# Kernel optimization log

Measured on AMD Instinct MI355X. Metric: run time of the kernel, lower is better.

The kernel has to match this reference:

```python
import jax, jax.numpy as jnp
import numpy as np

B, S, DIN, D, DOUT = 64, 128, 64, 1024, 64
NUM_ROTORS, NUM_REV = 3, 3


def setup_inputs() -> dict:
    key = jax.random.key(0)
    ks = jax.random.split(key, 12)
    s = 1.0 / np.sqrt(D)
    return {
        "x": jax.random.normal(ks[0], (B, S, DIN), jnp.float32),
        "Wi": jax.random.normal(ks[1], (D, DIN), jnp.float32) / np.sqrt(DIN),
        "bi": jnp.zeros((D,), jnp.float32),
        "P": jax.random.normal(ks[2], (D, D), jnp.float32) * s,          # plugboard
        "rotW": jax.random.normal(ks[3], (NUM_ROTORS, D, D), jnp.float32) * s,
        "F": jax.random.normal(ks[4], (NUM_REV, D // 2, D // 2), jnp.float32) * np.sqrt(2.0 / D),
        "G": jax.random.normal(ks[5], (NUM_REV, D // 2, D // 2), jnp.float32) * np.sqrt(2.0 / D),
        "R": jax.random.normal(ks[6], (D, D), jnp.float32) * (0.5 * s),  # reflector seed (symmetrized)
        "Wo": jax.random.normal(ks[7], (DOUT, D), jnp.float32) * s,
        "bo": jnp.zeros((DOUT,), jnp.float32),
    }


def _rev_block(h, f, g):
    # additive coupling (reversible block): split, couple, concat
    h1, h2 = jnp.split(h, 2, axis=-1)
    y1 = h1 + jnp.tanh(h2 @ f)
    y2 = h2 + jnp.tanh(y1 @ g)
    return jnp.concatenate([y1, y2], axis=-1)


def reference(x, Wi, bi, P, rotW, F, G, R, Wo, bo):
    d = Wi.shape[0]
    n_rot = rotW.shape[0]
    n_rev = F.shape[0]
    S_refl = R + R.T  # symmetric reflector

    def step(carry, inp):
        x_t, t = inp  # x_t: [B, DIN], t: scalar int32
        h = x_t @ Wi.T + bi                 # input projection
        h = h @ P.T                         # plugboard forward
        # rotors (odometer stepping: rotor i advances every d**i steps)
        for i in range(n_rot):
            pos = (t // (d ** i)) % d
            h = jnp.roll(jnp.roll(h, -pos, axis=-1) @ rotW[i], pos, axis=-1)
        for i in range(n_rev):
            h = _rev_block(h, F[i], G[i])
        h = h @ S_refl                      # reflector
        for i in reversed(range(n_rev)):
            h = _rev_block(h, F[i], G[i])
        for i in reversed(range(n_rot)):    # rotors inverse on return path
            pos = (t // (d ** i)) % d
            h = jnp.roll(jnp.roll(h, -pos, axis=-1) @ rotW[i].T, pos, axis=-1)
        h = h @ P                           # plugboard transpose
        return carry, h @ Wo.T + bo

    xs = (jnp.swapaxes(x, 0, 1), jnp.arange(x.shape[1], dtype=jnp.int32))
    _, outs = jax.lax.scan(step, 0, xs)     # outs: [S, B, DOUT]
    return jnp.swapaxes(outs, 0, 1)
```

## Files before the change

kernel.cpp:

```cpp
#include <hip/hip_runtime.h>
#include <math.h>

#define DD 1024
#define MM 8192
#define SS 128
#define DINN 64
#define DOUTN 64

typedef _Float16 f16;
typedef _Float16 f16x8 __attribute__((ext_vector_type(8)));
typedef _Float16 f16x4 __attribute__((ext_vector_type(4)));
typedef float    f32x4 __attribute__((ext_vector_type(4)));

#define GLOAD_LDS(g, l) \
  __builtin_amdgcn_global_load_lds((const __attribute__((address_space(1))) void*)(g), \
                                   (__attribute__((address_space(3))) void*)(l), 16, 0, 0)

template<int BM, bool EPI, int SHIFT>
__global__ __launch_bounds__(256)
void k_gemm16(const f16* __restrict__ A, int lda,
              const f16* __restrict__ B, int ldb,
              f16* __restrict__ C, int ldc, int K) {
  constexpr int MT = BM / 32;
  constexpr int AI = BM / 64;
  __shared__ f16 sA[2][BM * 32];
  __shared__ f16 sB[2][128 * 32];

  const int nwg = gridDim.x * gridDim.y;
  int wg = blockIdx.y * gridDim.x + blockIdx.x;
  wg = (wg & 7) * (nwg >> 3) + (wg >> 3);
  const int bx = wg % gridDim.x, by = wg / gridDim.x;

  const int col0 = bx * 128, row0 = by * BM;
  const int u = threadIdx.x, lane = u & 63, wv = u >> 6;
  const int mh = (wv >> 1) * (BM >> 1);
  const int nh = (wv & 1) * 64;

  unsigned aoff[AI], boff[2];
  unsigned dstA[AI], dstB[2];
#pragma unroll
  for (int i = 0; i < AI; ++i) {
    const int P = i * 256 + u;
    const int row = P >> 2, kc = (P & 3) ^ ((row >> 1) & 3);
    aoff[i] = (unsigned)(row0 + row) * lda + kc * 8;
    dstA[i] = (i * 256 + wv * 64) * 8;
  }
#pragma unroll
  for (int i = 0; i < 2; ++i) {
    const int P = i * 256 + u;
    const int row = P >> 2, kc = (P & 3) ^ ((row >> 1) & 3);
    boff[i] = (unsigned)(col0 + row) * ldb + kc * 8;
    dstB[i] = (i * 256 + wv * 64) * 8;
  }

  const int frag = (lane & 15) * 32 + (((lane >> 4) ^ ((lane >> 1) & 3)) * 8);

  f32x4 acc[MT][4];
#pragma unroll
  for (int i = 0; i < MT; ++i)
#pragma unroll
    for (int j = 0; j < 4; ++j) acc[i][j] = (f32x4){0.f, 0.f, 0.f, 0.f};

  auto stage = [&](int b, int k0) {
#pragma unroll
    for (int i = 0; i < AI; ++i)
      GLOAD_LDS(A + aoff[i] + k0, &sA[b][dstA[i]]);
#pragma unroll
    for (int i = 0; i < 2; ++i)
      GLOAD_LDS(B + boff[i] + k0, &sB[b][dstB[i]]);
  };

  const int niter = K >> 5;
  stage(0, 0);
  __syncthreads();

  int buf = 0;
  for (int it = 0; it < niter; ++it) {
    if (it + 1 < niter) stage(buf ^ 1, (it + 1) << 5);
    f16x8 aF[MT], bF[4];
#pragma unroll
    for (int mt = 0; mt < MT; ++mt)
      aF[mt] = *(const f16x8*)&sA[buf][(mh + mt * 16) * 32 + frag];
#pragma unroll
    for (int nt = 0; nt < 4; ++nt)
      bF[nt] = *(const f16x8*)&sB[buf][(nh + nt * 16) * 32 + frag];
#pragma unroll
    for (int mt = 0; mt < MT; ++mt)
#pragma unroll
      for (int nt = 0; nt < 4; ++nt)
        acc[mt][nt] = __builtin_amdgcn_mfma_f32_16x16x32_f16(aF[mt], bF[nt], acc[mt][nt], 0, 0, 0);
    __syncthreads();
    buf ^= 1;
  }

  if constexpr (SHIFT == 0) {
    f16* eH = &sB[0][0] + wv * (16 * 84);
    const int lrow4 = (lane >> 4) << 2;
    const int lcol = lane & 15;
#pragma unroll
    for (int mt = 0; mt < MT; ++mt) {
#pragma unroll
      for (int nt = 0; nt < 4; ++nt) {
        const f32x4 a = acc[mt][nt];
#pragma unroll
        for (int r = 0; r < 4; ++r)
          eH[(lrow4 + r) * 84 + nt * 16 + lcol] = (f16)a[r];
      }
#pragma unroll
      for (int j = 0; j < 2; ++j) {
        const int idx = j * 64 + lane;
        const int row = idx >> 3, ch = idx & 7;
        const f16x8 vh = *(const f16x8*)&eH[row * 84 + ch * 8];
        const int m = row0 + mh + mt * 16 + row;
        const size_t gi = (size_t)m * ldc + col0 + nh + ch * 8;
        if (EPI) {
          const f16x8 oh = *(const f16x8*)&C[gi];
          f16x8 rh;
#pragma unroll
          for (int q = 0; q < 8; ++q)
            rh[q] = (f16)((float)oh[q] + tanhf((float)vh[q]));
          *(f16x8*)&C[gi] = rh;
        } else {
          *(f16x8*)&C[gi] = vh;
        }
      }
    }
  } else {
#pragma unroll
    for (int mt = 0; mt < MT; ++mt)
#pragma unroll
      for (int nt = 0; nt < 4; ++nt) {
        const f32x4 a = acc[mt][nt];
        const int n_base = col0 + nh + nt * 16 + (lane & 15);
#pragma unroll
        for (int r = 0; r < 4; ++r) {
          const int m = row0 + mh + mt * 16 + ((lane >> 4) << 2) + r;
          int n = (n_base + SHIFT * (m >> 6) + 2048) & (DD - 1);
          const size_t idx = (size_t)m * ldc + n;
          float y = a[r];
          if (EPI) y = (float)C[idx] + tanhf(y);
          C[idx] = (f16)y;
        }
      }
  }
}

__global__ __launch_bounds__(256)
void k_in_mfma(const f16* __restrict__ xS,
               const f16* __restrict__ A2,
               const float* __restrict__ cvec,
               f16* __restrict__ hS) {
  __shared__ f16 sA[2][64 * 32];
  __shared__ f16 sB[2][128 * 32];
  const int bx = blockIdx.x, by = blockIdx.y;
  const int col0 = bx * 128, row0 = by * 64, t = by;
  const int u = threadIdx.x, lane = u & 63, wv = u >> 6;
  const int mh = (wv >> 1) * 32;
  const int nh = (wv & 1) * 64;

  unsigned aoff, boff[2], dstA, dstB[2];
  {
    const int row = u >> 2, kc = (u & 3) ^ ((row >> 1) & 3);
    aoff = (unsigned)(row * SS + t) * DINN + kc * 8;
    dstA = (unsigned)(wv * 64) * 8;
  }
#pragma unroll
  for (int i = 0; i < 2; ++i) {
    const int P = i * 256 + u;
    const int row = P >> 2, kc = (P & 3) ^ ((row >> 1) & 3);
    const int src = (col0 + row + t) & (DD - 1);
    boff[i] = (unsigned)src * DINN + kc * 8;
    dstB[i] = (i * 256 + wv * 64) * 8;
  }

  const int frag = (lane & 15) * 32 + (((lane >> 4) ^ ((lane >> 1) & 3)) * 8);

  f32x4 acc[2][4];
#pragma unroll
  for (int i = 0; i < 2; ++i)
#pragma unroll
    for (int j = 0; j < 4; ++j) acc[i][j] = (f32x4){0.f, 0.f, 0.f, 0.f};

  auto stage = [&](int b, int k0) {
    GLOAD_LDS(xS + aoff + k0, &sA[b][dstA]);
#pragma unroll
    for (int i = 0; i < 2; ++i)
      GLOAD_LDS(A2 + boff[i] + k0, &sB[b][dstB[i]]);
  };

  stage(0, 0);
  __syncthreads();
  int buf = 0;
#pragma unroll
  for (int it = 0; it < 2; ++it) {
    if (it == 0) stage(1, 32);
    f16x8 aF[2], bF[4];
#pragma unroll
    for (int mt = 0; mt < 2; ++mt)
      aF[mt] = *(const f16x8*)&sA[buf][(mh + mt * 16) * 32 + frag];
#pragma unroll
    for (int nt = 0; nt < 4; ++nt)
      bF[nt] = *(const f16x8*)&sB[buf][(nh + nt * 16) * 32 + frag];
#pragma unroll
    for (int mt = 0; mt < 2; ++mt)
#pragma unroll
      for (int nt = 0; nt < 4; ++nt)
        acc[mt][nt] = __builtin_amdgcn_mfma_f32_16x16x32_f16(aF[mt], bF[nt], acc[mt][nt], 0, 0, 0);
    __syncthreads();
    buf ^= 1;
  }

  f16* eH = &sB[0][0] + wv * (16 * 84);
  const int lrow4 = (lane >> 4) << 2;
  const int lcol = lane & 15;
#pragma unroll
  for (int mt = 0; mt < 2; ++mt) {
#pragma unroll
    for (int nt = 0; nt < 4; ++nt) {
      const f32x4 a = acc[mt][nt];
      const int n = col0 + nh + nt * 16 + lcol;
      const float cv = cvec[(n + t) & (DD - 1)];
#pragma unroll
      for (int r = 0; r < 4; ++r)
        eH[(lrow4 + r) * 84 + nt * 16 + lcol] = (f16)(a[r] + cv);
    }
#pragma unroll
    for (int j = 0; j < 2; ++j) {
      const int idx = j * 64 + lane;
      const int row = idx >> 3, ch = idx & 7;
      const f16x8 vh = *(const f16x8*)&eH[row * 84 + ch * 8];
      const int m = row0 + mh + mt * 16 + row;
      *(f16x8*)&hS[(size_t)m * DD + col0 + nh + ch * 8] = vh;
    }
  }
}

__global__ __launch_bounds__(256)
void k_out_mfma(const f16* __restrict__ A,
                const f16* __restrict__ B,
                const float* __restrict__ bo, float* __restrict__ out) {
  __shared__ f16 sA[2][64 * 32];
  __shared__ f16 sB[2][64 * 32];
  const int row0 = blockIdx.x * 64;
  const int u = threadIdx.x, lane = u & 63, wv = u >> 6;
  const int mh = (wv >> 1) * 32, nh = (wv & 1) * 32;

  const int srow = u >> 2, skc = (u & 3) ^ ((srow >> 1) & 3);
  const unsigned aoff = (unsigned)(row0 + srow) * DD + skc * 8;
  const unsigned boff = (unsigned)srow * DD + skc * 8;
  const unsigned dst = (unsigned)(wv * 64) * 8;

  const int frag = (lane & 15) * 32 + (((lane >> 4) ^ ((lane >> 1) & 3)) * 8);

  f32x4 acc[2][2];
#pragma unroll
  for (int i = 0; i < 2; ++i)
#pragma unroll
    for (int j = 0; j < 2; ++j) acc[i][j] = (f32x4){0.f, 0.f, 0.f, 0.f};

  auto stage = [&](int b, int k0) {
    GLOAD_LDS(A + aoff + k0, &sA[b][dst]);
    GLOAD_LDS(B + boff + k0, &sB[b][dst]);
  };

  stage(0, 0);
  __syncthreads();
  int buf = 0;
  for (int it = 0; it < 32; ++it) {
    if (it + 1 < 32) stage(buf ^ 1, (it + 1) << 5);
    f16x8 aF[2], bF[2];
#pragma unroll
    for (int mt = 0; mt < 2; ++mt)
      aF[mt] = *(const f16x8*)&sA[buf][(mh + mt * 16) * 32 + frag];
#pragma unroll
    for (int nt = 0; nt < 2; ++nt)
      bF[nt] = *(const f16x8*)&sB[buf][(nh + nt * 16) * 32 + frag];
#pragma unroll
    for (int mt = 0; mt < 2; ++mt)
#pragma unroll
      for (int nt = 0; nt < 2; ++nt)
        acc[mt][nt] = __builtin_amdgcn_mfma_f32_16x16x32_f16(aF[mt], bF[nt], acc[mt][nt], 0, 0, 0);
    __syncthreads();
    buf ^= 1;
  }

#pragma unroll
  for (int mt = 0; mt < 2; ++mt)
#pragma unroll
    for (int nt = 0; nt < 2; ++nt) {
      const f32x4 a = acc[mt][nt];
      const int c = nh + nt * 16 + (lane & 15);
      const float bias = bo[c];
#pragma unroll
      for (int r = 0; r < 4; ++r) {
        const int m = row0 + mh + mt * 16 + ((lane >> 4) << 2) + r;
        const int t = m >> 6, b = m & 63;
        out[((size_t)b * SS + t) * DOUTN + c] = a[r] + bias;
      }
    }
}

__global__ __launch_bounds__(256)
void k_cvt(const float* __restrict__ src, f16* __restrict__ dst) {
  const int i = blockIdx.x * 256 + threadIdx.x;
  const float4 v = ((const float4*)src)[i];
  f16x4 h4;
  h4[0] = (f16)v.x; h4[1] = (f16)v.y; h4[2] = (f16)v.z; h4[3] = (f16)v.w;
  ((f16x4*)dst)[i] = h4;
}

__global__ __launch_bounds__(256)
void k_cvtT(const float* __restrict__ src, f16* __restrict__ dst, int dim) {
  src += (size_t)blockIdx.z * dim * dim;
  dst += (size_t)blockIdx.z * dim * dim;
  const int i0 = blockIdx.y * 64, j0 = blockIdx.x * 64;
  __shared__ float tb[64][68];
  const int u = threadIdx.x;
#pragma unroll
  for (int it = 0; it < 4; ++it) {
    const int idx = it * 256 + u, rr = idx >> 4, cc = (idx & 15) * 4;
    *(float4*)&tb[rr][cc] = *(const float4*)&src[(size_t)(i0 + rr) * dim + j0 + cc];
  }
  __syncthreads();
#pragma unroll
  for (int it = 0; it < 4; ++it) {
    const int idx = it * 256 + u, rr = idx >> 4, cc = (idx & 15) * 4;
    f16x4 h4;
#pragma unroll
    for (int j = 0; j < 4; ++j) h4[j] = (f16)tb[cc + j][rr];
    *(f16x4*)&dst[(size_t)(j0 + rr) * dim + i0 + cc] = h4;
  }
}

__global__ __launch_bounds__(256)
void k_symm_cvt(const float* __restrict__ R, f16* __restrict__ S) {
  const int i0 = blockIdx.y * 64, j0 = blockIdx.x * 64;
  __shared__ float tb[64][68];
  const int u = threadIdx.x;
#pragma unroll
  for (int it = 0; it < 4; ++it) {
    const int idx = it * 256 + u, rr = idx >> 4, cc = (idx & 15) * 4;
    *(float4*)&tb[rr][cc] = *(const float4*)&R[(size_t)(j0 + rr) * DD + i0 + cc];
  }
  __syncthreads();
#pragma unroll
  for (int it = 0; it < 4; ++it) {
    const int idx = it * 256 + u, rr = idx >> 4, cc = (idx & 15) * 4;
    const float4 v = *(const float4*)&R[(size_t)(i0 + rr) * DD + j0 + cc];
    f16x4 h4;
    h4[0] = (f16)(v.x + tb[cc + 0][rr]); h4[1] = (f16)(v.y + tb[cc + 1][rr]);
    h4[2] = (f16)(v.z + tb[cc + 2][rr]); h4[3] = (f16)(v.w + tb[cc + 3][rr]);
    *(f16x4*)&S[(size_t)(i0 + rr) * DD + j0 + cc] = h4;
  }
}

__global__ __launch_bounds__(256)
void k_tr16(const f16* __restrict__ in, f16* __restrict__ o, int dim) {
  const int i0 = blockIdx.y * 64, j0 = blockIdx.x * 64;
  __shared__ f16 tb[64][72];
  const int u = threadIdx.x;
#pragma unroll
  for (int it = 0; it < 2; ++it) {
    const int C = it * 256 + u, row = C >> 3, ch = C & 7;
    *(f16x8*)&tb[row][ch * 8] = *(const f16x8*)&in[(size_t)(i0 + row) * dim + j0 + ch * 8];
  }
  __syncthreads();
#pragma unroll
  for (int it = 0; it < 2; ++it) {
    const int C = it * 256 + u, row = C >> 3, ch = C & 7;
    f16x8 v;
#pragma unroll
    for (int j = 0; j < 8; ++j) v[j] = tb[ch * 8 + j][row];
    *(f16x8*)&o[(size_t)(j0 + row) * dim + i0 + ch * 8] = v;
  }
}

__global__ __launch_bounds__(256)
void k_pwi(const float* __restrict__ P, const float* __restrict__ Wi,
           f16* __restrict__ A2) {
  const int m0 = blockIdx.x * 4;
  __shared__ float Ps[4][1024];
  const int u = threadIdx.x;
#pragma unroll
  for (int i = 0; i < 4; ++i) {
    const int idx = i * 256 + u, mi = idx >> 8, kc = (idx & 255) * 4;
    *(float4*)&Ps[mi][kc] = *(const float4*)&P[(size_t)(m0 + mi) * DD + kc];
  }
  __syncthreads();
  const int n = u & 63, mi = u >> 6;
  float acc = 0.f;
  for (int k = 0; k < DD; ++k) acc += Ps[mi][k] * Wi[(size_t)k * DINN + n];
  A2[(size_t)(m0 + mi) * DINN + n] = (f16)acc;
}

__global__ __launch_bounds__(256)
void k_pwo(const float* __restrict__ P, const float* __restrict__ Wo_,
           f16* __restrict__ MoT) {
  const int d0 = blockIdx.x * 4;
  __shared__ float Ps[4][1024];
  __shared__ float ws[64][65];
  const int u = threadIdx.x;
#pragma unroll
  for (int i = 0; i < 4; ++i) {
    const int idx = i * 256 + u, mi = idx >> 8, kc = (idx & 255) * 4;
    *(float4*)&Ps[mi][kc] = *(const float4*)&P[(size_t)(d0 + mi) * DD + kc];
  }
  const int c = u & 63, di = u >> 6;
  float acc = 0.f;
  for (int k0 = 0; k0 < DD; k0 += 64) {
    __syncthreads();
#pragma unroll
    for (int i = 0; i < 4; ++i) {
      const int idx = i * 256 + u, cc = idx >> 4, kc = (idx & 15) * 4;
      const float4 v = *(const float4*)&Wo_[(size_t)cc * DD + k0 + kc];
      ws[cc][kc] = v.x; ws[cc][kc + 1] = v.y; ws[cc][kc + 2] = v.z; ws[cc][kc + 3] = v.w;
    }
    __syncthreads();
    for (int kk = 0; kk < 64; ++kk) acc += Ps[di][k0 + kk] * ws[c][kk];
  }
  MoT[(size_t)c * DD + d0 + di] = (f16)acc;
}

__global__ __launch_bounds__(256)
void k_matvec(const float* __restrict__ P, const float* __restrict__ b,
              float* __restrict__ c) {
  const int row = blockIdx.x * 4 + (threadIdx.x >> 6);
  const int l = threadIdx.x & 63;
  float s = 0.f;
  for (int k = l; k < DD; k += 64) s += P[(size_t)row * DD + k] * b[k];
  for (int o = 32; o; o >>= 1) s += __shfl_down(s, o, 64);
  if (l == 0) c[row] = s;
}

extern "C" void kernel_launch(void* const* d_in, const int* in_sizes, int n_in,
                              void* d_out, int out_size, void* d_ws, size_t ws_size,
                              hipStream_t stream) {
  (void)in_sizes; (void)n_in; (void)out_size; (void)ws_size;
  const float* x    = (const float*)d_in[0];
  const float* Wi   = (const float*)d_in[1];
  const float* bi   = (const float*)d_in[2];
  const float* P    = (const float*)d_in[3];
  const float* rotW = (const float*)d_in[4];
  const float* F    = (const float*)d_in[5];
  const float* G    = (const float*)d_in[6];
  const float* R    = (const float*)d_in[7];
  const float* Wo   = (const float*)d_in[8];
  const float* bo   = (const float*)d_in[9];
  float* out = (float*)d_out;
  char* w = (char*)d_ws;

  constexpr size_t MB = 1u << 20;
  f16* haS = (f16*)(w + 0 * MB);
  f16* hbS = (f16*)(w + 16 * MB);
  f16* B0t = (f16*)(w + 32 * MB);
  f16* B12t= (f16*)(w + 34 * MB);
  f16* Bss = (f16*)(w + 36 * MB);
  f16* B12 = (f16*)(w + 38 * MB);
  f16* B0  = (f16*)(w + 40 * MB);
  f16* BF  = (f16*)(w + 42 * MB);
  f16* BG  = (f16*)(w + 44 * MB);
  f16* MoT    = (f16*)(w + 46 * MB);
  f16* A2     = (f16*)(w + 46 * MB + 128 * 1024);
  float* cvec = (float*)(w + 46 * MB + 256 * 1024);
  f16* xs     = (f16*)(w + 47 * MB);
  f16* W1s = (f16*)(w + 48 * MB);
  f16* W2t = (f16*)(w + 50 * MB);

  const float* W0 = rotW;
  const float* W1 = rotW + (1u << 20);
  const float* W2 = rotW + (2u << 20);

  const dim3 blk256(256);
  const size_t FGQ = (size_t)512 * 512;

  k_cvt     <<<dim3(1024), blk256, 0, stream>>>(W1, W1s);
  k_cvtT    <<<dim3(16, 16), blk256, 0, stream>>>(W2, W2t, DD);
  k_gemm16<64, false, 0><<<dim3(8, 16), blk256, 0, stream>>>(W1s, DD, W2t, DD, B12, DD, DD);
  k_tr16    <<<dim3(16, 16), blk256, 0, stream>>>(B12, B12t, DD);
  k_symm_cvt<<<dim3(16, 16), blk256, 0, stream>>>(R, Bss);
  k_cvtT    <<<dim3(16, 16), blk256, 0, stream>>>(W0, B0t, DD);
  k_cvt     <<<dim3(1024), blk256, 0, stream>>>(W0, B0);
  k_cvtT    <<<dim3(8, 8, 3), blk256, 0, stream>>>(F, BF, 512);
  k_cvtT    <<<dim3(8, 8, 3), blk256, 0, stream>>>(G, BG, 512);
  k_cvt     <<<dim3(512), blk256, 0, stream>>>(x, xs);
  k_pwi     <<<dim3(256), blk256, 0, stream>>>(P, Wi, A2);
  k_pwo     <<<dim3(256), blk256, 0, stream>>>(P, Wo, MoT);
  k_matvec  <<<dim3(256), blk256, 0, stream>>>(P, bi, cvec);

  k_in_mfma<<<dim3(8, 128), blk256, 0, stream>>>(xs, A2, cvec, haS);

  k_gemm16<128, false, +1><<<dim3(8, 64), blk256, 0, stream>>>(haS, DD, B0t, DD, hbS, DD, DD);
  k_gemm16<128, false, 0><<<dim3(8, 64), blk256, 0, stream>>>(hbS, DD, B12t, DD, haS, DD, DD);
  for (int i = 0; i < 3; ++i) {
    k_gemm16<64, true, 0><<<dim3(4, 128), blk256, 0, stream>>>(haS + 512, DD, BF + i * FGQ, 512, haS, DD, 512);
    k_gemm16<64, true, 0><<<dim3(4, 128), blk256, 0, stream>>>(haS, DD, BG + i * FGQ, 512, haS + 512, DD, 512);
  }
  k_gemm16<128, false, 0><<<dim3(8, 64), blk256, 0, stream>>>(haS, DD, Bss, DD, hbS, DD, DD);
  for (int i = 2; i >= 0; --i) {
    k_gemm16<64, true, 0><<<dim3(4, 128), blk256, 0, stream>>>(hbS + 512, DD, BF + i * FGQ, 512, hbS, DD, 512);
    k_gemm16<64, true, 0><<<dim3(4, 128), blk256, 0, stream>>>(hbS, DD, BG + i * FGQ, 512, hbS + 512, DD, 512);
  }
  k_gemm16<128, false, -1><<<dim3(8, 64), blk256, 0, stream>>>(hbS, DD, B12, DD, haS, DD, DD);
  k_gemm16<128, false, +1><<<dim3(8, 64), blk256, 0, stream>>>(haS, DD, B0, DD, hbS, DD, DD);

  k_out_mfma<<<dim3(128), blk256, 0, stream>>>(hbS, MoT, bo, out);
}
```

Baseline: 419.8 us.

## Split-K the W1·W2 precompute, merge conversion kernels, shrink main GEMM tiles

Merges several fp32-to-fp16 conversion and transpose launches into fewer combined kernels, which cuts launch count in the weight-prep phase. Replaces the 128-block W1·W2 product with a 4-way split-K GEMM into fp32 partials plus a summing kernel, giving that step more parallelism. Also switches the main 1024-wide GEMMs from BM=128 to BM=64 tiles, doubling the block count (1024 blocks) to improve CU occupancy at the cost of reloading the B operand more often. The split-K path adds 16 MB of fp32 partial traffic.

```diff
diff --git a/kernel.cpp b/kernel.cpp
--- a/kernel.cpp
+++ b/kernel.cpp
@@ -143,6 +143,94 @@
         }
       }
   }
+}
+
+__global__ __launch_bounds__(256)
+void k_w12part(const f16* __restrict__ A, const f16* __restrict__ B,
+               float* __restrict__ Cp) {
+  __shared__ f16 sA[2][64 * 32];
+  __shared__ f16 sB[2][128 * 32];
+  const int kOff = blockIdx.z * 256;
+  float* Co = Cp + (size_t)blockIdx.z * DD * DD;
+  const int col0 = blockIdx.x * 128, row0 = blockIdx.y * 64;
+  const int u = threadIdx.x, lane = u & 63, wv = u >> 6;
+  const int mh = (wv >> 1) * 32, nh = (wv & 1) * 64;
+
+  unsigned aoff, boff[2], dstA, dstB[2];
+  {
+    const int row = u >> 2, kc = (u & 3) ^ ((row >> 1) & 3);
+    aoff = (unsigned)(row0 + row) * DD + kOff + kc * 8;
+    dstA = (unsigned)(wv * 64) * 8;
+  }
+#pragma unroll
+  for (int i = 0; i < 2; ++i) {
+    const int P = i * 256 + u;
+    const int row = P >> 2, kc = (P & 3) ^ ((row >> 1) & 3);
+    boff[i] = (unsigned)(col0 + row) * DD + kOff + kc * 8;
+    dstB[i] = (i * 256 + wv * 64) * 8;
+  }
+  const int frag = (lane & 15) * 32 + (((lane >> 4) ^ ((lane >> 1) & 3)) * 8);
+
+  f32x4 acc[2][4];
+#pragma unroll
+  for (int i = 0; i < 2; ++i)
+#pragma unroll
+    for (int j = 0; j < 4; ++j) acc[i][j] = (f32x4){0.f, 0.f, 0.f, 0.f};
+
+  auto stage = [&](int b, int k0) {
+    GLOAD_LDS(A + aoff + k0, &sA[b][dstA]);
+#pragma unroll
+    for (int i = 0; i < 2; ++i)
+      GLOAD_LDS(B + boff[i] + k0, &sB[b][dstB[i]]);
+  };
+
+  stage(0, 0);
+  __syncthreads();
+  int buf = 0;
+  for (int it = 0; it < 8; ++it) {
+    if (it + 1 < 8) stage(buf ^ 1, (it + 1) << 5);
+    f16x8 aF[2], bF[4];
+#pragma unroll
+    for (int mt = 0; mt < 2; ++mt)
+      aF[mt] = *(const f16x8*)&sA[buf][(mh + mt * 16) * 32 + frag];
+#pragma unroll
+    for (int nt = 0; nt < 4; ++nt)
+      bF[nt] = *(const f16x8*)&sB[buf][(nh + nt * 16) * 32 + frag];
+#pragma unroll
+    for (int mt = 0; mt < 2; ++mt)
+#pragma unroll
+      for (int nt = 0; nt < 4; ++nt)
+        acc[mt][nt] = __builtin_amdgcn_mfma_f32_16x16x32_f16(aF[mt], bF[nt], acc[mt][nt], 0, 0, 0);
+    __syncthreads();
+    buf ^= 1;
+  }
+#pragma unroll
+  for (int mt = 0; mt < 2; ++mt)
+#pragma unroll
+    for (int nt = 0; nt < 4; ++nt) {
+      const f32x4 a = acc[mt][nt];
+      const int n = col0 + nh + nt * 16 + (lane & 15);
+#pragma unroll
+      for (int r = 0; r < 4; ++r) {
+        const int m = row0 + mh + mt * 16 + ((lane >> 4) << 2) + r;
+        Co[(size_t)m * DD + n] = a[r];
+      }
+    }
+}
+
+__global__ __launch_bounds__(256)
+void k_sum4(const float* __restrict__ Wp, f16* __restrict__ B12) {
+  const int i = blockIdx.x * 256 + threadIdx.x;
+  const float4 s0 = ((const float4*)Wp)[i];
+  const float4 s1 = ((const float4*)(Wp + (1u << 20)))[i];
+  const float4 s2 = ((const float4*)(Wp + (2u << 20)))[i];
+  const float4 s3 = ((const float4*)(Wp + (3u << 20)))[i];
+  f16x4 h4;
+  h4[0] = (f16)(s0.x + s1.x + s2.x + s3.x);
+  h4[1] = (f16)(s0.y + s1.y + s2.y + s3.y);
+  h4[2] = (f16)(s0.z + s1.z + s2.z + s3.z);
+  h4[3] = (f16)(s0.w + s1.w + s2.w + s3.w);
+  ((f16x4*)B12)[i] = h4;
 }
 
 __global__ __launch_bounds__(256)
@@ -301,25 +389,32 @@
 }
 
 __global__ __launch_bounds__(256)
-void k_cvt(const float* __restrict__ src, f16* __restrict__ dst) {
+void k_cvt_all(const float* __restrict__ W1, const float* __restrict__ W0,
+               const float* __restrict__ x,
+               f16* __restrict__ W1s, f16* __restrict__ B0, f16* __restrict__ xs) {
   const int i = blockIdx.x * 256 + threadIdx.x;
-  const float4 v = ((const float4*)src)[i];
+  const float* src; f16* dst; int j;
+  if (i < 262144)      { src = W1; dst = W1s; j = i; }
+  else if (i < 524288) { src = W0; dst = B0;  j = i - 262144; }
+  else                 { src = x;  dst = xs;  j = i - 524288; }
+  const float4 v = ((const float4*)src)[j];
   f16x4 h4;
   h4[0] = (f16)v.x; h4[1] = (f16)v.y; h4[2] = (f16)v.z; h4[3] = (f16)v.w;
-  ((f16x4*)dst)[i] = h4;
-}
-
-__global__ __launch_bounds__(256)
-void k_cvtT(const float* __restrict__ src, f16* __restrict__ dst, int dim) {
-  src += (size_t)blockIdx.z * dim * dim;
-  dst += (size_t)blockIdx.z * dim * dim;
+  ((f16x4*)dst)[j] = h4;
+}
+
+__global__ __launch_bounds__(256)
+void k_cvtT2(const float* __restrict__ s0, f16* __restrict__ d0,
+             const float* __restrict__ s1, f16* __restrict__ d1) {
+  const float* src = blockIdx.z ? s1 : s0;
+  f16* dst = blockIdx.z ? d1 : d0;
   const int i0 = blockIdx.y * 64, j0 = blockIdx.x * 64;
   __shared__ float tb[64][68];
   const int u = threadIdx.x;
 #pragma unroll
   for (int it = 0; it < 4; ++it) {
     const int idx = it * 256 + u, rr = idx >> 4, cc = (idx & 15) * 4;
-    *(float4*)&tb[rr][cc] = *(const float4*)&src[(size_t)(i0 + rr) * dim + j0 + cc];
+    *(float4*)&tb[rr][cc] = *(const float4*)&src[(size_t)(i0 + rr) * DD + j0 + cc];
   }
   __syncthreads();
 #pragma unroll
@@ -328,7 +423,33 @@
     f16x4 h4;
 #pragma unroll
     for (int j = 0; j < 4; ++j) h4[j] = (f16)tb[cc + j][rr];
-    *(f16x4*)&dst[(size_t)(j0 + rr) * dim + i0 + cc] = h4;
+    *(f16x4*)&dst[(size_t)(j0 + rr) * DD + i0 + cc] = h4;
+  }
+}
+
+__global__ __launch_bounds__(256)
+void k_cvtT_fg(const float* __restrict__ F, const float* __restrict__ G,
+               f16* __restrict__ BF, f16* __restrict__ BG) {
+  const int z = blockIdx.z;
+  const size_t off = (size_t)(z % 3) * 512 * 512;
+  const float* src = (z < 3 ? F : G) + off;
+  f16* dst = (z < 3 ? BF : BG) + off;
+  const int i0 = blockIdx.y * 64, j0 = blockIdx.x * 64;
+  __shared__ float tb[64][68];
+  const int u = threadIdx.x;
+#pragma unroll
+  for (int it = 0; it < 4; ++it) {
+    const int idx = it * 256 + u, rr = idx >> 4, cc = (idx & 15) * 4;
+    *(float4*)&tb[rr][cc] = *(const float4*)&src[(size_t)(i0 + rr) * 512 + j0 + cc];
+  }
+  __syncthreads();
+#pragma unroll
+  for (int it = 0; it < 4; ++it) {
+    const int idx = it * 256 + u, rr = idx >> 4, cc = (idx & 15) * 4;
+    f16x4 h4;
+#pragma unroll
+    for (int j = 0; j < 4; ++j) h4[j] = (f16)tb[cc + j][rr];
+    *(f16x4*)&dst[(size_t)(j0 + rr) * 512 + i0 + cc] = h4;
   }
 }
 
@@ -465,6 +586,7 @@
   f16* xs     = (f16*)(w + 47 * MB);
   f16* W1s = (f16*)(w + 48 * MB);
   f16* W2t = (f16*)(w + 50 * MB);
+  float* Wp = (float*)(w + 52 * MB);
 
   const float* W0 = rotW;
   const float* W1 = rotW + (1u << 20);
@@ -473,35 +595,32 @@
   const dim3 blk256(256);
   const size_t FGQ = (size_t)512 * 512;
 
-  k_cvt     <<<dim3(1024), blk256, 0, stream>>>(W1, W1s);
-  k_cvtT    <<<dim3(16, 16), blk256, 0, stream>>>(W2, W2t, DD);
-  k_gemm16<64, false, 0><<<dim3(8, 16), blk256, 0, stream>>>(W1s, DD, W2t, DD, B12, DD, DD);
+  k_cvt_all <<<dim3(2560), blk256, 0, stream>>>(W1, W0, x, W1s, B0, xs);
+  k_cvtT2   <<<dim3(16, 16, 2), blk256, 0, stream>>>(W2, W2t, W0, B0t);
+  k_cvtT_fg <<<dim3(8, 8, 6), blk256, 0, stream>>>(F, G, BF, BG);
+  k_symm_cvt<<<dim3(16, 16), blk256, 0, stream>>>(R, Bss);
+  k_w12part <<<dim3(8, 16, 4), blk256, 0, stream>>>(W1s, W2t, Wp);
+  k_sum4    <<<dim3(1024), blk256, 0, stream>>>(Wp, B12);
   k_tr16    <<<dim3(16, 16), blk256, 0, stream>>>(B12, B12t, DD);
-  k_symm_cvt<<<dim3(16, 16), blk256, 0, stream>>>(R, Bss);
-  k_cvtT    <<<dim3(16, 16), blk256, 0, stream>>>(W0, B0t, DD);
-  k_cvt     <<<dim3(1024), blk256, 0, stream>>>(W0, B0);
-  k_cvtT    <<<dim3(8, 8, 3), blk256, 0, stream>>>(F, BF, 512);
-  k_cvtT    <<<dim3(8, 8, 3), blk256, 0, stream>>>(G, BG, 512);
-  k_cvt     <<<dim3(512), blk256, 0, stream>>>(x, xs);
   k_pwi     <<<dim3(256), blk256, 0, stream>>>(P, Wi, A2);
   k_pwo     <<<dim3(256), blk256, 0, stream>>>(P, Wo, MoT);
   k_matvec  <<<dim3(256), blk256, 0, stream>>>(P, bi, cvec);
 
   k_in_mfma<<<dim3(8, 128), blk256, 0, stream>>>(xs, A2, cvec, haS);
 
-  k_gemm16<128, false, +1><<<dim3(8, 64), blk256, 0, stream>>>(haS, DD, B0t, DD, hbS, DD, DD);
-  k_gemm16<128, false, 0><<<dim3(8, 64), blk256, 0, stream>>>(hbS, DD, B12t, DD, haS, DD, DD);
+  k_gemm16<64, false, +1><<<dim3(8, 128), blk256, 0, stream>>>(haS, DD, B0t, DD, hbS, DD, DD);
+  k_gemm16<64, false, 0><<<dim3(8, 128), blk256, 0, stream>>>(hbS, DD, B12t, DD, haS, DD, DD);
   for (int i = 0; i < 3; ++i) {
     k_gemm16<64, true, 0><<<dim3(4, 128), blk256, 0, stream>>>(haS + 512, DD, BF + i * FGQ, 512, haS, DD, 512);
     k_gemm16<64, true, 0><<<dim3(4, 128), blk256, 0, stream>>>(haS, DD, BG + i * FGQ, 512, haS + 512, DD, 512);
   }
-  k_gemm16<128, false, 0><<<dim3(8, 64), blk256, 0, stream>>>(haS, DD, Bss, DD, hbS, DD, DD);
+  k_gemm16<64, false, 0><<<dim3(8, 128), blk256, 0, stream>>>(haS, DD, Bss, DD, hbS, DD, DD);
   for (int i = 2; i >= 0; --i) {
     k_gemm16<64, true, 0><<<dim3(4, 128), blk256, 0, stream>>>(hbS + 512, DD, BF + i * FGQ, 512, hbS, DD, 512);
     k_gemm16<64, true, 0><<<dim3(4, 128), blk256, 0, stream>>>(hbS, DD, BG + i * FGQ, 512, hbS + 512, DD, 512);
   }
-  k_gemm16<128, false, -1><<<dim3(8, 64), blk256, 0, stream>>>(hbS, DD, B12, DD, haS, DD, DD);
-  k_gemm16<128, false, +1><<<dim3(8, 64), blk256, 0, stream>>>(haS, DD, B0, DD, hbS, DD, DD);
+  k_gemm16<64, false, -1><<<dim3(8, 128), blk256, 0, stream>>>(hbS, DD, B12, DD, haS, DD, DD);
+  k_gemm16<64, false, +1><<<dim3(8, 128), blk256, 0, stream>>>(haS, DD, B0, DD, hbS, DD, DD);
 
   k_out_mfma<<<dim3(128), blk256, 0, stream>>>(hbS, MoT, bo, out);
 }
```

After: 401.3 us. -4.4%, faster.
